# Kernel tuning notes

Measured on AMD Instinct MI355X. Metric: run time of the kernel, lower is better.

The kernel has to match this reference:

```python
import jax, jax.numpy as jnp
import numpy as np

TEMP = 0.07   # config['temperature']
EPS = 1e-8    # torch cosine-similarity eps
NEG_INF = -1e30


def _l2norm(x):
    return x / jnp.maximum(jnp.linalg.norm(x, axis=-1, keepdims=True), EPS)


def _remove_diag(m):
    # [n,n] -> [n,n-1], drop the diagonal of each row (extract_non_diagonal_matrix)
    n = m.shape[0]
    return m.reshape(-1)[:-1].reshape(n - 1, n + 1)[:, 1:].reshape(n, n - 1)


def _contrastive(e1, e2):
    # NT-Xent between two views, compared across the batch at matched temporal
    # positions (finegrain=False path). e1, e2: [b, s, d]
    b = e1.shape[0]
    z = jnp.concatenate([e1.transpose(1, 0, 2), e2.transpose(1, 0, 2)], axis=1)  # [s, 2b, d]
    zn = _l2norm(z)
    sim = jnp.einsum('pnd,pmd->pnm', zn, zn) / TEMP  # [s, 2b, 2b]
    pos = jnp.concatenate([
        jnp.diagonal(sim, b, axis1=-2, axis2=-1),
        jnp.diagonal(sim, -b, axis1=-2, axis2=-1),
    ], axis=1)  # [s, 2b]
    N = 2 * b
    eyeb = jnp.eye(b, dtype=bool)
    excl = jnp.eye(N, dtype=bool)
    excl = excl.at[:b, b:].set(excl[:b, b:] | eyeb).at[b:, :b].set(excl[b:, :b] | eyeb)
    neg = jnp.where(~excl, sim, NEG_INF)  # [s, 2b, 2b], 2b-2 live entries/row
    logits = jnp.concatenate([pos[..., None], neg], axis=-1)
    # CrossEntropyLoss(label=0), mean
    return jnp.mean(jax.nn.logsumexp(logits, axis=-1) - pos)


def _coarse_temporal(f):
    # samples within a sequence = positives, other sequences = negatives
    b, s, d = f.shape
    zn = _l2norm(f.reshape(b * s, d))
    sim = (zn @ zn.T) / TEMP  # [bs, bs]
    # diagonal over the batch blocks -> [b, s, s]
    sim_ii = jnp.diagonal(sim.reshape(b, s, b, s), axis1=0, axis2=2).transpose(2, 0, 1)
    pos = jax.vmap(_remove_diag)(sim_ii).reshape(b * s, s - 1)
    blk = jnp.repeat(jnp.repeat(~jnp.eye(b, dtype=bool), s, axis=0), s, axis=1)
    neg = jnp.where(blk, sim, NEG_INF)  # (b-1)*s live entries per row
    logits = jnp.concatenate([pos, neg], axis=1)
    return jnp.mean(jax.nn.logsumexp(logits, axis=1) - logits[:, 0])


def _ortho(x1, x2):
    # CosineEmbeddingLoss with target=-1, margin=0: mean(relu(cos(x1, x2)))
    a = _l2norm(x1.reshape(-1, x1.shape[-1]))
    b = _l2norm(x2.reshape(-1, x2.shape[-1]))
    return jnp.mean(jax.nn.relu(jnp.sum(a * b, axis=-1)))


def _forward(mod1_v1, mod1_v2, mod2_v1, mod2_v2, seq_len):
    d = mod1_v1.shape[-1]
    h = d // 2
    f1 = [mod1_v1.reshape(-1, seq_len, d), mod2_v1.reshape(-1, seq_len, d)]  # view 1, per mod
    f2 = [mod1_v2.reshape(-1, seq_len, d), mod2_v2.reshape(-1, seq_len, d)]  # view 2, per mod
    sh = lambda x: x[..., :h]
    pv = lambda x: x[..., h:]

    # (2) shared contrastive between modalities, per view
    shared_loss = _contrastive(sh(f1[0]), sh(f1[1])) + _contrastive(sh(f2[0]), sh(f2[1]))
    # (3) private contrastive between views, per modality
    private_loss = _contrastive(pv(f1[0]), pv(f2[0])) + _contrastive(pv(f1[1]), pv(f2[1]))
    # (4) orthogonality: shared-vs-private per mod per view, private-vs-private per view
    ortho_loss = (_ortho(sh(f1[0]), pv(f1[0])) + _ortho(sh(f1[1]), pv(f1[1]))
                  + _ortho(sh(f2[0]), pv(f2[0])) + _ortho(sh(f2[1]), pv(f2[1]))
                  + _ortho(pv(f1[0]), pv(f1[1])) + _ortho(pv(f2[0]), pv(f2[1])))
    # (5) temporal consistency: coarse temporal contrastive per mod per view
    temporal_loss = (_coarse_temporal(f1[0]) + _coarse_temporal(f1[1])
                     + _coarse_temporal(f2[0]) + _coarse_temporal(f2[1]))
    return shared_loss + private_loss + ortho_loss + temporal_loss


def setup_inputs() -> dict:
    key = jax.random.key(0)
    ks = jax.random.split(key, 4)
    B, S, D = 512, 8, 128
    return {
        'mod1_v1': jax.random.normal(ks[0], (B * S, D), dtype=jnp.float32),
        'mod1_v2': jax.random.normal(ks[1], (B * S, D), dtype=jnp.float32),
        'mod2_v1': jax.random.normal(ks[2], (B * S, D), dtype=jnp.float32),
        'mod2_v2': jax.random.normal(ks[3], (B * S, D), dtype=jnp.float32),
        'seq_len': S,
    }


def reference(mod1_v1, mod1_v2, mod2_v1, mod2_v2, seq_len):
    return _forward(mod1_v1, mod1_v2, mod2_v1, mod2_v2, seq_len)
```

## Files before the change

kernel.cpp:

```cpp
#include <hip/hip_runtime.h>
#include <math.h>

#define CTR_L1 0
#define CTR_L2 2048
#define RS_T   49152
#define RS_C   65536
#define SLOT   98304
#define ZF_BYTE 397312
#define ZH_BYTE 4591616

#define INV_T 14.285714285714286f
#define C1EXP 20.609929155556627f
#define EPS_N 1e-8f
#define NBLK_TAIL 192

typedef __attribute__((ext_vector_type(8))) short short8;
typedef __attribute__((ext_vector_type(4))) float floatx4;

__device__ __forceinline__ const float* pick4(const float* a, const float* b,
                                              const float* c, const float* d, int i) {
    return i == 0 ? a : i == 1 ? b : i == 2 ? c : d;
}

__device__ __forceinline__ unsigned short f2bf(float x) {
    unsigned u = __float_as_uint(x);
    u += 0x7fff + ((u >> 16) & 1);
    return (unsigned short)(u >> 16);
}

__global__ __launch_bounds__(256) void k_prep(const float* __restrict__ in0, const float* __restrict__ in1,
                                              const float* __restrict__ in2, const float* __restrict__ in3,
                                              float* __restrict__ ws) {
    __shared__ float buf[4][8][128];
    __shared__ float iv[3][32];
    __shared__ float red[3];
    const int s = blockIdx.x;
    const int tid = threadIdx.x;

    int gid = s * 256 + tid;
    if (gid < 2080) ws[gid] = 0.0f;
    if (gid < 50176) ws[RS_T + gid] = 0.0f;
    if (tid < 3) red[tid] = 0.0f;

    #pragma unroll
    for (int i = 0; i < 4; i++) {
        int e4 = tid + i * 256;
        int inp = e4 >> 8, row = (e4 >> 5) & 7, c4 = e4 & 31;
        float4 f = *(const float4*)(pick4(in0, in1, in2, in3, inp) + (size_t)(s * 8 + row) * 128 + c4 * 4);
        *(float4*)(&buf[inp][row][c4 * 4]) = f;
    }
    __syncthreads();

    {
        int row32 = tid >> 3, seg = tid & 7;
        const float* rp_ = &buf[row32 >> 3][row32 & 7][seg * 16];
        float ss = 0.0f;
        #pragma unroll
        for (int k = 0; k < 4; k++) {
            float4 x = *(const float4*)(rp_ + k * 4);
            ss = fmaf(x.x, x.x, fmaf(x.y, x.y, fmaf(x.z, x.z, fmaf(x.w, x.w, ss))));
        }
        ss += __shfl_xor(ss, 1); ss += __shfl_xor(ss, 2);
        float cross = __shfl_xor(ss, 4);
        if (seg == 0) {
            iv[0][row32] = 1.0f / fmaxf(sqrtf(ss), EPS_N);
            iv[2][row32] = 1.0f / fmaxf(sqrtf(ss + cross), EPS_N);
        }
        if (seg == 4) iv[1][row32] = 1.0f / fmaxf(sqrtf(ss), EPS_N);
    }
    __syncthreads();

    {
        int input = tid >> 6, row = (tid >> 3) & 7, kc0 = (tid & 7) * 2;
        int rg = s * 8 + row;
        float scF = iv[2][input * 8 + row];
        unsigned short* zf = (unsigned short*)((char*)ws + ZF_BYTE) + (size_t)input * 524288
                           + ((rg >> 4) * 16) * 128 + (rg & 15) * 8;
        unsigned short* zh = (unsigned short*)((char*)ws + ZH_BYTE) + (size_t)input * 524288
                           + row * 65536 + ((s >> 4) * 16) * 128 + (s & 15) * 8;
        #pragma unroll
        for (int kk = 0; kk < 2; kk++) {
            int kc = kc0 + kk;
            float scH = iv[kc < 8 ? 0 : 1][input * 8 + row];
            const float* bp = &buf[input][row][kc * 8];
            float4 x = *(const float4*)bp;
            float4 y = *(const float4*)(bp + 4);
            ushort4 f0, f1, h0, h1;
            f0.x = f2bf(x.x * scF); f0.y = f2bf(x.y * scF); f0.z = f2bf(x.z * scF); f0.w = f2bf(x.w * scF);
            f1.x = f2bf(y.x * scF); f1.y = f2bf(y.y * scF); f1.z = f2bf(y.z * scF); f1.w = f2bf(y.w * scF);
            h0.x = f2bf(x.x * scH); h0.y = f2bf(x.y * scH); h0.z = f2bf(x.z * scH); h0.w = f2bf(x.w * scH);
            h1.x = f2bf(y.x * scH); h1.y = f2bf(y.y * scH); h1.z = f2bf(y.z * scH); h1.w = f2bf(y.w * scH);
            *(ushort4*)(zf + kc * 128)     = f0;
            *(ushort4*)(zf + kc * 128 + 4) = f1;
            *(ushort4*)(zh + kc * 128)     = h0;
            *(ushort4*)(zh + kc * 128 + 4) = h1;
        }
    }

    float val = 0.0f;
    int cat = -1;
    if (tid < 48) {
        const int oa[6]  = {0, 2, 1, 3, 0, 1};
        const int oaf[6] = {0, 0, 0, 0, 64, 64};
        const int ob[6]  = {0, 2, 1, 3, 2, 3};
        int term = tid >> 3, row = tid & 7;
        const float* A = &buf[oa[term]][row][oaf[term]];
        const float* B = &buf[ob[term]][row][64];
        float d = 0.0f;
        #pragma unroll
        for (int k = 0; k < 16; k++) {
            float4 x = *(const float4*)(A + k * 4);
            float4 y = *(const float4*)(B + k * 4);
            d = fmaf(x.x, y.x, fmaf(x.y, y.y, fmaf(x.z, y.z, fmaf(x.w, y.w, d))));
        }
        float ia = iv[oaf[term] ? 1 : 0][oa[term] * 8 + row];
        float ib = iv[1][ob[term] * 8 + row];
        val = fmaxf(d * ia * ib, 0.0f);
        cat = 2;
    } else if (tid < 80) {
        const int ca[4] = {0, 1, 0, 2}, cb[4] = {2, 3, 1, 3}, coff[4] = {0, 0, 64, 64};
        int call = (tid - 48) >> 3, row = (tid - 48) & 7;
        const float* A = &buf[ca[call]][row][coff[call]];
        const float* B = &buf[cb[call]][row][coff[call]];
        float d = 0.0f;
        #pragma unroll
        for (int k = 0; k < 16; k++) {
            float4 x = *(const float4*)(A + k * 4);
            float4 y = *(const float4*)(B + k * 4);
            d = fmaf(x.x, y.x, fmaf(x.y, y.y, fmaf(x.z, y.z, fmaf(x.w, y.w, d))));
        }
        int ivb = coff[call] ? 1 : 0;
        val = d * iv[ivb][ca[call] * 8 + row] * iv[ivb][cb[call] * 8 + row];
        cat = 0;
    } else if (tid < 136) {
        int u = tid - 80;
        int inp = u / 14, v = u % 14, pp = v >> 1, half = v & 1;
        int ra = (pp == 0) ? 1 : (pp + 1);
        const float* A = &buf[inp][ra][half * 64];
        const float* B = &buf[inp][0][half * 64];
        float d = 0.0f;
        #pragma unroll
        for (int k = 0; k < 16; k++) {
            float4 x = *(const float4*)(A + k * 4);
            float4 y = *(const float4*)(B + k * 4);
            d = fmaf(x.x, y.x, fmaf(x.y, y.y, fmaf(x.z, y.z, fmaf(x.w, y.w, d))));
        }
        float wgt = (pp == 0) ? 2.0f : 1.0f;
        val = d * wgt * iv[2][inp * 8 + ra] * iv[2][inp * 8];
        cat = 1;
    }
    if (cat >= 0) atomicAdd(&red[cat], val);
    __syncthreads();
    if (tid == 0) atomicAdd(ws + SLOT + 32 * 24, red[0]);
    if (tid == 1) atomicAdd(ws + SLOT + 32 * 25, red[1]);
    if (tid == 2) atomicAdd(ws + SLOT + 32 * (16 + (s & 7)), red[2]);
}

__global__ __launch_bounds__(256, 4) void k_gram(float* __restrict__ ws) {
    const int tid = threadIdx.x;
    const int b = blockIdx.x;
    const int w = tid >> 6, lane = tid & 63, quad = (tid >> 4) & 3, l15 = tid & 15;
    const int wrow = (w >> 1) * 64, wcol = (w & 1) * 64;
    const int laneoff = (lane >> 4) * 128 + (lane & 15) * 8;

    const short* aPtr;
    const short* bPtr;
    int nk;
    float* rsR;
    float* rsC;
    bool diag;

    if (b < 2176) {
        int input = b / 544, t = b % 544;
        int j = t >> 5, i = t & 31;
        if (j == 16 && i >= 16) return;
        int rt = i, ct = (i + j) & 31;
        diag = (j == 0);
        const short* zf = (const short*)((const char*)ws + ZF_BYTE) + (size_t)input * 524288;
        aPtr = zf + (rt * 8 + (wrow >> 4)) * 2048 + laneoff;
        bPtr = zf + (ct * 8 + (wcol >> 4)) * 2048 + laneoff;
        nk = 2;
        rsR = ws + RS_T + input * 4096 + rt * 128;
        rsC = ws + RS_T + input * 4096 + ct * 128;
    } else {
        int c = b - 2176;
        int callp = c / 40, t = c % 40;
        int j = t >> 3, i = t & 7;
        if (j == 4 && i >= 4) return;
        int call = callp >> 3, p = callp & 7;
        int rt = i, ct = (i + j) & 7;
        diag = (j == 0);
        const int ca[4] = {0, 1, 0, 2}, cb[4] = {2, 3, 1, 3};
        const int hb = (call >= 2) ? 8 : 0;
        const short* zh = (const short*)((const char*)ws + ZH_BYTE);
        int rbase = rt * 128, cbase = ct * 128;
        aPtr = zh + (size_t)(rbase < 512 ? ca[call] : cb[call]) * 524288 + p * 65536
                  + ((((rbase & 511) >> 4) + (wrow >> 4)) * 16 + hb) * 128 + laneoff;
        bPtr = zh + (size_t)(cbase < 512 ? ca[call] : cb[call]) * 524288 + p * 65536
                  + ((((cbase & 511) >> 4) + (wcol >> 4)) * 16 + hb) * 128 + laneoff;
        nk = 1;
        rsR = ws + RS_C + (call * 8 + p) * 1024 + rbase;
        rsC = ws + RS_C + (call * 8 + p) * 1024 + cbase;
    }

    floatx4 acc[4][4];
    #pragma unroll
    for (int ri = 0; ri < 4; ri++)
        #pragma unroll
        for (int ci = 0; ci < 4; ci++) acc[ri][ci] = (floatx4){0.f, 0.f, 0.f, 0.f};

    for (int kh = 0; kh < nk; kh++) {
        #pragma unroll
        for (int ks = 0; ks < 2; ks++) {
            const int koff = (kh * 8 + ks * 4) * 128;
            short8 a[4], bb[4];
            #pragma unroll
            for (int i = 0; i < 4; i++) {
                a[i]  = *(const short8*)(aPtr + i * 2048 + koff);
                bb[i] = *(const short8*)(bPtr + i * 2048 + koff);
            }
            #pragma unroll
            for (int ri = 0; ri < 4; ri++)
                #pragma unroll
                for (int ci = 0; ci < 4; ci++)
                    acc[ri][ci] = __builtin_amdgcn_mfma_f32_16x16x32_bf16(a[ri], bb[ci], acc[ri][ci], 0, 0, 0);
        }
    }

    if (diag) {
        #pragma unroll
        for (int ri = 0; ri < 4; ri++) {
            #pragma unroll
            for (int reg = 0; reg < 4; reg++) {
                int rloc = wrow + ri * 16 + quad * 4 + reg;
                float rp = 0.f;
                #pragma unroll
                for (int ci = 0; ci < 4; ci++) {
                    int cloc = wcol + ci * 16 + l15;
                    float ex = __builtin_amdgcn_exp2f(fmaf(acc[ri][ci][reg], C1EXP, -C1EXP));
                    rp += (cloc != rloc) ? ex : 0.f;
                }
                rp += __shfl_xor(rp, 1); rp += __shfl_xor(rp, 2);
                rp += __shfl_xor(rp, 4); rp += __shfl_xor(rp, 8);
                if (l15 == 0) atomicAdd(rsR + rloc, rp);
            }
        }
    } else {
        float colp[4] = {0.f, 0.f, 0.f, 0.f};
        #pragma unroll
        for (int ri = 0; ri < 4; ri++) {
            #pragma unroll
            for (int reg = 0; reg < 4; reg++) {
                int rloc = wrow + ri * 16 + quad * 4 + reg;
                float rp = 0.f;
                #pragma unroll
                for (int ci = 0; ci < 4; ci++) {
                    float ex = __builtin_amdgcn_exp2f(fmaf(acc[ri][ci][reg], C1EXP, -C1EXP));
                    rp += ex;
                    colp[ci] += ex;
                }
                rp += __shfl_xor(rp, 1); rp += __shfl_xor(rp, 2);
                rp += __shfl_xor(rp, 4); rp += __shfl_xor(rp, 8);
                if (l15 == 0) atomicAdd(rsR + rloc, rp);
            }
        }
        #pragma unroll
        for (int ci = 0; ci < 4; ci++) {
            colp[ci] += __shfl_xor(colp[ci], 16);
            colp[ci] += __shfl_xor(colp[ci], 32);
            if (lane < 16) atomicAdd(rsC + wcol + ci * 16 + l15, colp[ci]);
        }
    }
}

__global__ __launch_bounds__(256) void k_tail(float* __restrict__ ws, float* __restrict__ out) {
    __shared__ float tred[4];
    __shared__ int lastf;
    const int tid = threadIdx.x;
    const int b = blockIdx.x;
    const int idx = b * 256 + tid;

    float l = __logf(ws[RS_T + idx]);
    #pragma unroll
    for (int m = 1; m < 64; m <<= 1) l += __shfl_xor(l, m);
    if ((tid & 63) == 0) tred[tid >> 6] = l;
    __syncthreads();
    if (tid == 0) {
        float bs = tred[0] + tred[1] + tred[2] + tred[3];
        int slot = (idx < 16384) ? (8 + (b & 7)) : (b & 7);
        atomicAdd(ws + SLOT + 32 * slot, bs);
    }
    __syncthreads();
    if (tid == 0) {
        int last = 0;
        int o1 = __hip_atomic_fetch_add((int*)(ws + CTR_L1 + 32 * (b & 7)), 1,
                                        __ATOMIC_RELAXED, __HIP_MEMORY_SCOPE_AGENT);
        if (o1 == 23) {
            int o2 = __hip_atomic_fetch_add((int*)(ws + CTR_L2), 1,
                                            __ATOMIC_RELAXED, __HIP_MEMORY_SCOPE_AGENT);
            last = (o2 == 7);
        }
        lastf = last;
    }
    __syncthreads();
    if (!lastf) return;

    if (tid < 64) {
        float v2 = 0.0f;
        if (tid < 26) {
            float x = __hip_atomic_load(ws + SLOT + 32 * tid, __ATOMIC_RELAXED, __HIP_MEMORY_SCOPE_AGENT);
            float wgt;
            if (tid < 8)       wgt = 1.0f / 8192.0f;
            else if (tid < 24) wgt = 1.0f / 4096.0f;
            else if (tid == 24) wgt = -2.0f * INV_T / 8192.0f;
            else                wgt = -INV_T / 4096.0f;
            v2 = x * wgt;
        }
        #pragma unroll
        for (int m = 1; m < 64; m <<= 1) v2 += __shfl_xor(v2, m);
        if (tid == 0) out[0] = v2 + 8.0f * INV_T;
    }
}

extern "C" void kernel_launch(void* const* d_in, const int* in_sizes, int n_in,
                              void* d_out, int out_size, void* d_ws, size_t ws_size,
                              hipStream_t stream) {
    (void)in_sizes; (void)n_in; (void)out_size; (void)ws_size;
    const float* in0 = (const float*)d_in[0];
    const float* in1 = (const float*)d_in[1];
    const float* in2 = (const float*)d_in[2];
    const float* in3 = (const float*)d_in[3];
    float* ws = (float*)d_ws;
    float* out = (float*)d_out;

    hipLaunchKernelGGL(k_prep, dim3(512), dim3(256), 0, stream, in0, in1, in2, in3, ws);
    hipLaunchKernelGGL(k_gram, dim3(3456), dim3(256), 0, stream, ws);
    hipLaunchKernelGGL(k_tail, dim3(NBLK_TAIL), dim3(256), 0, stream, ws, out);
}
```

Baseline: 131.4 us.

## Give each gram block several column tiles and restructure bf16 conversion in prep

k_gram now has each block keep one row tile and loop over several column tiles, reusing the row-tile A fragments. Row-sum partials stay in registers and are written with one set of atomics at the end, which cuts block count and row atomics. The bf16 normalization and layout writes move into 128 dedicated prep blocks that read rows straight from global memory. Launch bounds drop to 3 waves per SIMD, trading occupancy for more registers, and work per block is now uneven (2–5 tiles).

```diff
diff --git a/kernel.cpp b/kernel.cpp
--- a/kernel.cpp
+++ b/kernel.cpp
@@ -28,15 +28,70 @@
     return (unsigned short)(u >> 16);
 }
 
+__device__ __forceinline__ ushort4 cvt4(float4 x, float sc) {
+    ushort4 o;
+    o.x = f2bf(x.x * sc); o.y = f2bf(x.y * sc); o.z = f2bf(x.z * sc); o.w = f2bf(x.w * sc);
+    return o;
+}
+
 __global__ __launch_bounds__(256) void k_prep(const float* __restrict__ in0, const float* __restrict__ in1,
                                               const float* __restrict__ in2, const float* __restrict__ in3,
                                               float* __restrict__ ws) {
+    __shared__ float ivf[128], ivs[128], ivp[128];
     __shared__ float buf[4][8][128];
     __shared__ float iv[3][32];
     __shared__ float red[3];
-    const int s = blockIdx.x;
     const int tid = threadIdx.x;
-
+    const int blk = blockIdx.x;
+
+    if (blk < 128) {
+        const int input = blk >> 5, g = blk & 31;
+        const float* src = pick4(in0, in1, in2, in3, input) + (size_t)(g * 128) * 128;
+        {
+            int r = tid >> 1, half = tid & 1;
+            const float* rp_ = src + r * 128 + half * 64;
+            float ss = 0.0f;
+            #pragma unroll
+            for (int k = 0; k < 16; k++) {
+                float4 x = *(const float4*)(rp_ + k * 4);
+                ss = fmaf(x.x, x.x, fmaf(x.y, x.y, fmaf(x.z, x.z, fmaf(x.w, x.w, ss))));
+            }
+            float other = __shfl_xor(ss, 1);
+            if (half == 0) {
+                ivs[r] = 1.0f / fmaxf(sqrtf(ss), EPS_N);
+                ivf[r] = 1.0f / fmaxf(sqrtf(ss + other), EPS_N);
+            } else {
+                ivp[r] = 1.0f / fmaxf(sqrtf(ss), EPS_N);
+            }
+        }
+        __syncthreads();
+        unsigned short* zf = (unsigned short*)((char*)ws + ZF_BYTE) + (size_t)input * 524288 + (size_t)g * 16384;
+        unsigned short* zh = (unsigned short*)((char*)ws + ZH_BYTE) + (size_t)input * 524288;
+        #pragma unroll
+        for (int k = 0; k < 8; k++) {
+            int ch = k * 256 + tid;
+            int lr = ((ch >> 8) << 4) | (ch & 15);
+            int kc = (ch >> 4) & 15;
+            const float* sp = src + lr * 128 + kc * 8;
+            float sc = ivf[lr];
+            *(ushort4*)(zf + ch * 8)     = cvt4(*(const float4*)sp, sc);
+            *(ushort4*)(zf + ch * 8 + 4) = cvt4(*(const float4*)(sp + 4), sc);
+        }
+        #pragma unroll
+        for (int k = 0; k < 8; k++) {
+            int ch = k * 256 + tid;
+            int p = ch >> 8, kc = (ch >> 4) & 15, slot = ch & 15;
+            int lr = slot * 8 + p;
+            const float* sp = src + lr * 128 + kc * 8;
+            float sc = (kc < 8 ? ivs : ivp)[lr];
+            unsigned short* dst = zh + (size_t)p * 65536 + (size_t)g * 2048 + (ch & 255) * 8;
+            *(ushort4*)dst       = cvt4(*(const float4*)sp, sc);
+            *(ushort4*)(dst + 4) = cvt4(*(const float4*)(sp + 4), sc);
+        }
+        return;
+    }
+
+    const int s = blk - 128;
     int gid = s * 256 + tid;
     if (gid < 2080) ws[gid] = 0.0f;
     if (gid < 50176) ws[RS_T + gid] = 0.0f;
@@ -50,7 +105,6 @@
         *(float4*)(&buf[inp][row][c4 * 4]) = f;
     }
     __syncthreads();
-
     {
         int row32 = tid >> 3, seg = tid & 7;
         const float* rp_ = &buf[row32 >> 3][row32 & 7][seg * 16];
@@ -69,33 +123,6 @@
         if (seg == 4) iv[1][row32] = 1.0f / fmaxf(sqrtf(ss), EPS_N);
     }
     __syncthreads();
-
-    {
-        int input = tid >> 6, row = (tid >> 3) & 7, kc0 = (tid & 7) * 2;
-        int rg = s * 8 + row;
-        float scF = iv[2][input * 8 + row];
-        unsigned short* zf = (unsigned short*)((char*)ws + ZF_BYTE) + (size_t)input * 524288
-                           + ((rg >> 4) * 16) * 128 + (rg & 15) * 8;
-        unsigned short* zh = (unsigned short*)((char*)ws + ZH_BYTE) + (size_t)input * 524288
-                           + row * 65536 + ((s >> 4) * 16) * 128 + (s & 15) * 8;
-        #pragma unroll
-        for (int kk = 0; kk < 2; kk++) {
-            int kc = kc0 + kk;
-            float scH = iv[kc < 8 ? 0 : 1][input * 8 + row];
-            const float* bp = &buf[input][row][kc * 8];
-            float4 x = *(const float4*)bp;
-            float4 y = *(const float4*)(bp + 4);
-            ushort4 f0, f1, h0, h1;
-            f0.x = f2bf(x.x * scF); f0.y = f2bf(x.y * scF); f0.z = f2bf(x.z * scF); f0.w = f2bf(x.w * scF);
-            f1.x = f2bf(y.x * scF); f1.y = f2bf(y.y * scF); f1.z = f2bf(y.z * scF); f1.w = f2bf(y.w * scF);
-            h0.x = f2bf(x.x * scH); h0.y = f2bf(x.y * scH); h0.z = f2bf(x.z * scH); h0.w = f2bf(x.w * scH);
-            h1.x = f2bf(y.x * scH); h1.y = f2bf(y.y * scH); h1.z = f2bf(y.z * scH); h1.w = f2bf(y.w * scH);
-            *(ushort4*)(zf + kc * 128)     = f0;
-            *(ushort4*)(zf + kc * 128 + 4) = f1;
-            *(ushort4*)(zh + kc * 128)     = h0;
-            *(ushort4*)(zh + kc * 128 + 4) = h1;
-        }
-    }
 
     float val = 0.0f;
     int cat = -1;
@@ -156,7 +183,7 @@
     if (tid == 2) atomicAdd(ws + SLOT + 32 * (16 + (s & 7)), red[2]);
 }
 
-__global__ __launch_bounds__(256, 4) void k_gram(float* __restrict__ ws) {
+__global__ __launch_bounds__(256, 3) void k_gram(float* __restrict__ ws) {
     const int tid = threadIdx.x;
     const int b = blockIdx.x;
     const int w = tid >> 6, lane = tid & 63, quad = (tid >> 4) & 3, l15 = tid & 15;
@@ -164,55 +191,68 @@
     const int laneoff = (lane >> 4) * 128 + (lane & 15) * 8;
 
     const short* aPtr;
-    const short* bPtr;
-    int nk;
+    const short* planeA;
+    const short* planeB;
+    int nk, ntiles, jbase, modm;
     float* rsR;
-    float* rsC;
-    bool diag;
-
-    if (b < 2176) {
-        int input = b / 544, t = b % 544;
-        int j = t >> 5, i = t & 31;
-        if (j == 16 && i >= 16) return;
-        int rt = i, ct = (i + j) & 31;
-        diag = (j == 0);
+    float* rsCbase;
+    bool temporal = (b < 1024);
+    int rt;
+
+    if (temporal) {
+        int input = b >> 8;
+        rt = (b >> 3) & 31;
+        int chunk = b & 7;
         const short* zf = (const short*)((const char*)ws + ZF_BYTE) + (size_t)input * 524288;
+        planeA = planeB = zf;
         aPtr = zf + (rt * 8 + (wrow >> 4)) * 2048 + laneoff;
-        bPtr = zf + (ct * 8 + (wcol >> 4)) * 2048 + laneoff;
-        nk = 2;
+        nk = 2; modm = 31;
+        jbase = chunk * 2;
+        ntiles = 2 + ((chunk == 7 && rt < 16) ? 1 : 0);
         rsR = ws + RS_T + input * 4096 + rt * 128;
-        rsC = ws + RS_T + input * 4096 + ct * 128;
+        rsCbase = ws + RS_T + input * 4096;
     } else {
-        int c = b - 2176;
-        int callp = c / 40, t = c % 40;
-        int j = t >> 3, i = t & 7;
-        if (j == 4 && i >= 4) return;
-        int call = callp >> 3, p = callp & 7;
-        int rt = i, ct = (i + j) & 7;
-        diag = (j == 0);
+        int c = b - 1024;
+        int call = c >> 6, p = (c >> 3) & 7;
+        rt = c & 7;
         const int ca[4] = {0, 1, 0, 2}, cb[4] = {2, 3, 1, 3};
         const int hb = (call >= 2) ? 8 : 0;
         const short* zh = (const short*)((const char*)ws + ZH_BYTE);
-        int rbase = rt * 128, cbase = ct * 128;
-        aPtr = zh + (size_t)(rbase < 512 ? ca[call] : cb[call]) * 524288 + p * 65536
-                  + ((((rbase & 511) >> 4) + (wrow >> 4)) * 16 + hb) * 128 + laneoff;
-        bPtr = zh + (size_t)(cbase < 512 ? ca[call] : cb[call]) * 524288 + p * 65536
-                  + ((((cbase & 511) >> 4) + (wcol >> 4)) * 16 + hb) * 128 + laneoff;
-        nk = 1;
-        rsR = ws + RS_C + (call * 8 + p) * 1024 + rbase;
-        rsC = ws + RS_C + (call * 8 + p) * 1024 + cbase;
-    }
-
-    floatx4 acc[4][4];
+        planeA = zh + (size_t)ca[call] * 524288 + (size_t)p * 65536 + hb * 128;
+        planeB = zh + (size_t)cb[call] * 524288 + (size_t)p * 65536 + hb * 128;
+        const short* rpl = (rt < 4) ? planeA : planeB;
+        aPtr = rpl + ((rt & 3) * 8 + (wrow >> 4)) * 2048 + laneoff;
+        nk = 1; modm = 7;
+        jbase = 0;
+        ntiles = (rt < 4) ? 5 : 4;
+        rsR = ws + RS_C + (call * 8 + p) * 1024 + rt * 128;
+        rsCbase = ws + RS_C + (call * 8 + p) * 1024;
+    }
+
+    float rp_acc[16];
     #pragma unroll
-    for (int ri = 0; ri < 4; ri++)
-        #pragma unroll
-        for (int ci = 0; ci < 4; ci++) acc[ri][ci] = (floatx4){0.f, 0.f, 0.f, 0.f};
-
-    for (int kh = 0; kh < nk; kh++) {
-        #pragma unroll
-        for (int ks = 0; ks < 2; ks++) {
-            const int koff = (kh * 8 + ks * 4) * 128;
+    for (int i = 0; i < 16; i++) rp_acc[i] = 0.0f;
+
+    for (int t = 0; t < ntiles; t++) {
+        int j = (temporal && t == 2) ? 16 : (jbase + t);
+        int ct = (rt + j) & modm;
+        bool diag = (j == 0);
+        const short* bPtr;
+        if (temporal) {
+            bPtr = planeA + (ct * 8 + (wcol >> 4)) * 2048 + laneoff;
+        } else {
+            const short* cpl = (ct < 4) ? planeA : planeB;
+            bPtr = cpl + ((ct & 3) * 8 + (wcol >> 4)) * 2048 + laneoff;
+        }
+
+        floatx4 acc[4][4];
+        #pragma unroll
+        for (int ri = 0; ri < 4; ri++)
+            #pragma unroll
+            for (int ci = 0; ci < 4; ci++) acc[ri][ci] = (floatx4){0.f, 0.f, 0.f, 0.f};
+
+        for (int ksb = 0; ksb < 2 * nk; ksb++) {
+            const int koff = ksb * 512;
             short8 a[4], bb[4];
             #pragma unroll
             for (int i = 0; i < 4; i++) {
@@ -225,50 +265,57 @@
                 for (int ci = 0; ci < 4; ci++)
                     acc[ri][ci] = __builtin_amdgcn_mfma_f32_16x16x32_bf16(a[ri], bb[ci], acc[ri][ci], 0, 0, 0);
         }
-    }
-
-    if (diag) {
-        #pragma unroll
-        for (int ri = 0; ri < 4; ri++) {
-            #pragma unroll
-            for (int reg = 0; reg < 4; reg++) {
-                int rloc = wrow + ri * 16 + quad * 4 + reg;
-                float rp = 0.f;
+
+        if (diag) {
+            #pragma unroll
+            for (int ri = 0; ri < 4; ri++) {
                 #pragma unroll
-                for (int ci = 0; ci < 4; ci++) {
-                    int cloc = wcol + ci * 16 + l15;
-                    float ex = __builtin_amdgcn_exp2f(fmaf(acc[ri][ci][reg], C1EXP, -C1EXP));
-                    rp += (cloc != rloc) ? ex : 0.f;
+                for (int reg = 0; reg < 4; reg++) {
+                    int rloc = wrow + ri * 16 + quad * 4 + reg;
+                    float rp = 0.f;
+                    #pragma unroll
+                    for (int ci = 0; ci < 4; ci++) {
+                        int cloc = wcol + ci * 16 + l15;
+                        float ex = __builtin_amdgcn_exp2f(fmaf(acc[ri][ci][reg], C1EXP, -C1EXP));
+                        rp += (cloc != rloc) ? ex : 0.f;
+                    }
+                    rp_acc[ri * 4 + reg] += rp;
                 }
-                rp += __shfl_xor(rp, 1); rp += __shfl_xor(rp, 2);
-                rp += __shfl_xor(rp, 4); rp += __shfl_xor(rp, 8);
-                if (l15 == 0) atomicAdd(rsR + rloc, rp);
-            }
-        }
-    } else {
-        float colp[4] = {0.f, 0.f, 0.f, 0.f};
-        #pragma unroll
-        for (int ri = 0; ri < 4; ri++) {
-            #pragma unroll
-            for (int reg = 0; reg < 4; reg++) {
-                int rloc = wrow + ri * 16 + quad * 4 + reg;
-                float rp = 0.f;
+            }
+        } else {
+            float colp[4] = {0.f, 0.f, 0.f, 0.f};
+            #pragma unroll
+            for (int ri = 0; ri < 4; ri++) {
                 #pragma unroll
-                for (int ci = 0; ci < 4; ci++) {
-                    float ex = __builtin_amdgcn_exp2f(fmaf(acc[ri][ci][reg], C1EXP, -C1EXP));
-                    rp += ex;
-                    colp[ci] += ex;
+                for (int reg = 0; reg < 4; reg++) {
+                    float rp = 0.f;
+                    #pragma unroll
+                    for (int ci = 0; ci < 4; ci++) {
+                        float ex = __builtin_amdgcn_exp2f(fmaf(acc[ri][ci][reg], C1EXP, -C1EXP));
+                        rp += ex;
+                        colp[ci] += ex;
+                    }
+                    rp_acc[ri * 4 + reg] += rp;
                 }
-                rp += __shfl_xor(rp, 1); rp += __shfl_xor(rp, 2);
-                rp += __shfl_xor(rp, 4); rp += __shfl_xor(rp, 8);
-                if (l15 == 0) atomicAdd(rsR + rloc, rp);
-            }
-        }
-        #pragma unroll
-        for (int ci = 0; ci < 4; ci++) {
-            colp[ci] += __shfl_xor(colp[ci], 16);
-            colp[ci] += __shfl_xor(colp[ci], 32);
-            if (lane < 16) atomicAdd(rsC + wcol + ci * 16 + l15, colp[ci]);
+            }
+            float* rsC = rsCbase + ct * 128;
+            #pragma unroll
+            for (int ci = 0; ci < 4; ci++) {
+                colp[ci] += __shfl_xor(colp[ci], 16);
+                colp[ci] += __shfl_xor(colp[ci], 32);
+                if (lane < 16) atomicAdd(rsC + wcol + ci * 16 + l15, colp[ci]);
+            }
+        }
+    }
+
+    #pragma unroll
+    for (int ri = 0; ri < 4; ri++) {
+        #pragma unroll
+        for (int reg = 0; reg < 4; reg++) {
+            float rp = rp_acc[ri * 4 + reg];
+            rp += __shfl_xor(rp, 1); rp += __shfl_xor(rp, 2);
+            rp += __shfl_xor(rp, 4); rp += __shfl_xor(rp, 8);
+            if (l15 == 0) atomicAdd(rsR + wrow + ri * 16 + quad * 4 + reg, rp);
         }
     }
 }
@@ -333,7 +380,7 @@
     float* ws = (float*)d_ws;
     float* out = (float*)d_out;
 
-    hipLaunchKernelGGL(k_prep, dim3(512), dim3(256), 0, stream, in0, in1, in2, in3, ws);
-    hipLaunchKernelGGL(k_gram, dim3(3456), dim3(256), 0, stream, ws);
+    hipLaunchKernelGGL(k_prep, dim3(640), dim3(256), 0, stream, in0, in1, in2, in3, ws);
+    hipLaunchKernelGGL(k_gram, dim3(1280), dim3(256), 0, stream, ws);
     hipLaunchKernelGGL(k_tail, dim3(NBLK_TAIL), dim3(256), 0, stream, ws, out);
 }
```

Result: faster. 114.3 us (median of 3 runs) (-13.0%).
